# Kernel optimization log

Hardware: AMD Instinct MI355X
Metric: run time of the kernel (lower is better)

Reference implementation:

```python
import jax, jax.numpy as jnp
import numpy as np

B, S, H = 4, 4096, 4096
E, G, TOPK_GROUP, TOP_K = 160, 8, 3, 6
SCALE = 16.0      # routed_scaling_factor (norm_topk_prob=False)
ALPHA = 0.001     # aux_loss_alpha
M = 3             # config.M for communication aux loss


def setup_inputs() -> dict:
    key = jax.random.key(0)
    k1, k2 = jax.random.split(key)
    hidden_states = jax.random.normal(k1, (B, S, H), dtype=jnp.float32)
    # kaiming_uniform_(a=sqrt(5)) on (E, H): bound = 1/sqrt(fan_in)
    bound = 1.0 / np.sqrt(H)
    weight = jax.random.uniform(k2, (E, H), minval=-bound, maxval=bound, dtype=jnp.float32)
    return {"hidden_states": hidden_states, "weight": weight}


def _gate(hidden_states, weight):
    b, s, h = hidden_states.shape
    x = hidden_states.reshape(-1, h).astype(jnp.float32)          # [T, H]
    logits = x @ weight.astype(jnp.float32).T                      # [T, E]
    scores = jax.nn.softmax(logits, axis=-1)
    T = b * s
    # group-limited greedy top-k
    group_scores = scores.reshape(T, G, E // G).max(axis=-1)       # [T, G]
    _, group_idx = jax.lax.top_k(group_scores, TOPK_GROUP)         # [T, topk_group]
    group_mask = jnp.zeros((T, G), scores.dtype).at[
        jnp.arange(T)[:, None], group_idx].set(1.0)                # [T, G]
    score_mask = jnp.repeat(group_mask, E // G, axis=1)            # [T, E]
    tmp_scores = jnp.where(score_mask > 0, scores, 0.0)
    topk_weight, topk_idx = jax.lax.top_k(tmp_scores, TOP_K)       # [T, k]
    topk_weight = topk_weight * SCALE
    # --- aux losses (training, seq_aux=True, alpha>0) ---
    idx_flat = topk_idx.reshape(b, s * TOP_K)                      # [b, s*k]
    counts = jax.vmap(
        lambda idx: jnp.zeros((E,), jnp.float32).at[idx].add(1.0)
    )(idx_flat)                                                    # [b, E]
    ce = counts / (s * TOP_K / E)
    mean_scores = scores.reshape(b, s, E).mean(axis=1)             # [b, E]
    aux_expert = (ce * mean_scores).sum(axis=1).mean() * ALPHA
    ce_g = ce.reshape(b, G, -1).mean(axis=-1)                      # [b, G]
    ms_g = mean_scores.reshape(b, G, -1).mean(axis=-1)             # [b, G]
    aux_device = (ce_g * ms_g).sum(axis=1).mean() * ALPHA
    ce2 = counts.reshape(b, G, -1).sum(axis=-1) / (M * s / G)      # [b, G]
    aux_comm = (ce2 * ms_g).sum(axis=1).mean() * ALPHA
    aux_loss = aux_expert + aux_device + aux_comm
    return topk_idx, topk_weight, aux_loss


def reference(hidden_states, weight):
    return _gate(hidden_states, weight)
```

## Files before the change

kernel.cpp:

```cpp
#include <hip/hip_runtime.h>

typedef _Float16 half8 __attribute__((ext_vector_type(8)));
typedef float f32x4 __attribute__((ext_vector_type(4)));

#define H    4096
#define NE   160
#define BM   64
#define TPB  512
#define NIT  64


__global__ __launch_bounds__(256) void prep_kernel(
    const float* __restrict__ w, _Float16* __restrict__ Wf)
{
    int F    = blockIdx.x * 256 + threadIdx.x;
    int lane = F & 63;
    int t10  = (F >> 6) % 10;
    int ks   = F / 640;
    int e    = t10 * 16 + (lane & 15);
    int k0   = ks * 32 + (lane >> 4) * 8;
    const float* p = w + (size_t)e * H + k0;
    float4 v0 = *(const float4*)p;
    float4 v1 = *(const float4*)(p + 4);
    float vv[8] = {v0.x, v0.y, v0.z, v0.w, v1.x, v1.y, v1.z, v1.w};
    half8 h0, h1;
#pragma unroll
    for (int j = 0; j < 8; ++j) {
        float s = vv[j] * 64.f;
        _Float16 a = (_Float16)s;
        h0[j] = a;
        h1[j] = (_Float16)((s - (float)a) * 2048.f);
    }
    half8* out = (half8*)Wf;
    out[(ks * 20 + t10) * 64 + lane]      = h0;
    out[(ks * 20 + 10 + t10) * 64 + lane] = h1;
}

#define GLOAD_LDS(SRC, DST)                                                    \
    __builtin_amdgcn_global_load_lds(                                          \
        (const __attribute__((address_space(1))) unsigned int*)(SRC),          \
        (__attribute__((address_space(3))) unsigned int*)(DST), 16, 0, 0)

#define LOADX(U0, U1, KIDX)                                                    \
    do {                                                                       \
        U0 = *(const float4*)(xp + (size_t)(KIDX) * 32);                       \
        U1 = *(const float4*)(xp + (size_t)(KIDX) * 32 + 4);                   \
    } while (0)

#define CONVERT(U0, U1)                                                        \
    do {                                                                       \
        float v0=U0.x, v1=U0.y, v2=U0.z, v3=U0.w;                              \
        float v4=U1.x, v5=U1.y, v6=U1.z, v7=U1.w;                              \
        _Float16 h;                                                            \
        h=(_Float16)v0; a0[0]=h; a1[0]=(_Float16)((v0-(float)h)*2048.f);       \
        h=(_Float16)v1; a0[1]=h; a1[1]=(_Float16)((v1-(float)h)*2048.f);       \
        h=(_Float16)v2; a0[2]=h; a1[2]=(_Float16)((v2-(float)h)*2048.f);       \
        h=(_Float16)v3; a0[3]=h; a1[3]=(_Float16)((v3-(float)h)*2048.f);       \
        h=(_Float16)v4; a0[4]=h; a1[4]=(_Float16)((v4-(float)h)*2048.f);       \
        h=(_Float16)v5; a0[5]=h; a1[5]=(_Float16)((v5-(float)h)*2048.f);       \
        h=(_Float16)v6; a0[6]=h; a1[6]=(_Float16)((v6-(float)h)*2048.f);       \
        h=(_Float16)v7; a0[7]=h; a1[7]=(_Float16)((v7-(float)h)*2048.f);       \
    } while (0)

#define KSTEP(LKS, U0, U1)                                                     \
    do {                                                                       \
        const half8* _B = (const half8*)s_stage + cur * 2560 + (LKS) * 1280    \
                          + nh * 5 * 64 + lane;                                \
        half8 bb0[5], bb1[5];                                                  \
        _Pragma("unroll")                                                      \
        for (int _t = 0; _t < 5; ++_t) {                                       \
            bb0[_t] = _B[_t * 64];                                             \
            bb1[_t] = _B[640 + _t * 64];                                       \
        }                                                                      \
        CONVERT(U0, U1);                                                       \
        _Pragma("unroll")                                                      \
        for (int _t = 0; _t < 5; ++_t) {                                       \
            accH[_t] = __builtin_amdgcn_mfma_f32_16x16x32_f16(a0, bb0[_t], accH[_t], 0, 0, 0); \
            accL[_t] = __builtin_amdgcn_mfma_f32_16x16x32_f16(a1, bb0[_t], accL[_t], 0, 0, 0); \
            accL[_t] = __builtin_amdgcn_mfma_f32_16x16x32_f16(a0, bb1[_t], accL[_t], 0, 0, 0); \
        }                                                                      \
    } while (0)

__global__ __launch_bounds__(TPB) void gate_kernel(
    const float* __restrict__ x, const _Float16* __restrict__ Wf,
    float* __restrict__ outIdx, float* __restrict__ outW,
    float* __restrict__ gcnt, float* __restrict__ gssum)
{
    __shared__ __align__(16) _Float16 s_stage[2 * 2560 * 8];
    __shared__ float s_mx[BM], s_inv[BM];
    __shared__ int   s_cnt[NE];
    float* s_log = (float*)s_stage;

    const int tid  = threadIdx.x;
    const int lane = tid & 63;
    const int wv   = tid >> 6;
    const int mh   = wv >> 1;
    const int nh   = wv & 1;
    const int row0 = blockIdx.x * BM;
    const int rowl = mh * 16 + (lane & 15);
    const int kq   = (lane >> 4) * 8;

    if (tid < NE) s_cnt[tid] = 0;

    f32x4 accH[5], accL[5];
#pragma unroll
    for (int t = 0; t < 5; ++t) { accH[t] = (f32x4){0,0,0,0}; accL[t] = (f32x4){0,0,0,0}; }

    const float* xp = x + (size_t)(row0 + rowl) * H + kq;

    half8 a0, a1;
    float4 uA0, uA1, uB0, uB1, uC0, uC1, uD0, uD1, uE0, uE1, uF0, uF1;

    {
        const _Float16* src = Wf + (size_t)tid * 8;
        _Float16*       dst = s_stage + (size_t)tid * 8;
#pragma unroll
        for (int i = 0; i < 5; ++i)
            GLOAD_LDS(src + i * 4096, dst + i * 4096);
    }
    LOADX(uA0, uA1, 0);
    LOADX(uB0, uB1, 1);
    LOADX(uC0, uC1, 2);
    LOADX(uD0, uD1, 3);
    asm volatile("s_waitcnt vmcnt(0)" ::: "memory");
    __syncthreads();

    int cur = 0;
    for (int it = 0; it < NIT; ++it) {
        if (it + 1 < NIT) {
            const _Float16* src = Wf + ((size_t)(it + 1) * 2560 + tid) * 8;
            _Float16*       dst = s_stage + ((size_t)(cur ^ 1) * 2560 + tid) * 8;
#pragma unroll
            for (int i = 0; i < 5; ++i)
                GLOAD_LDS(src + i * 4096, dst + i * 4096);
        }
        {
            const int kpa = ((it + 2) * 2) & (2 * NIT - 1);
            LOADX(uE0, uE1, kpa);
            LOADX(uF0, uF1, kpa + 1);
        }
        KSTEP(0, uA0, uA1);
        KSTEP(1, uB0, uB1);

        asm volatile("s_waitcnt vmcnt(0)" ::: "memory");
        __syncthreads();

        uA0 = uC0; uA1 = uC1; uB0 = uD0; uB1 = uD1;
        uC0 = uE0; uC1 = uE1; uD0 = uF0; uD1 = uF1;
        cur ^= 1;
    }

    const int crow  = mh * 16 + (lane >> 4) * 4;
    const int ccol0 = nh * 80 + (lane & 15);
#pragma unroll
    for (int t = 0; t < 5; ++t)
#pragma unroll
        for (int r = 0; r < 4; ++r)
            s_log[(crow + r) * 161 + ccol0 + t * 16] =
                (accH[t][r] + accL[t][r] * (1.0f / 2048.f)) * (1.0f / 64.f);
    __syncthreads();

    if (tid < BM) {
        const float* L = &s_log[tid * 161];
        float gmax[8];
        float mx = -3.4e38f;
#pragma unroll
        for (int g = 0; g < 8; ++g) {
            float m = L[g * 20];
            for (int j = 1; j < 20; ++j) m = fmaxf(m, L[g * 20 + j]);
            gmax[g] = m;
            mx = fmaxf(mx, m);
        }
        float sum = 0.f;
        for (int e = 0; e < NE; ++e) sum += __expf(L[e] - mx);
        float inv = 1.0f / sum;
        s_mx[tid]  = mx;
        s_inv[tid] = inv;

        unsigned sel = 0;
        float pv = 3.4e38f; int pi = -1;
        for (int it = 0; it < 3; ++it) {
            float bv = -3.4e38f; int bi = 0;
            for (int g = 0; g < 8; ++g) {
                float v = gmax[g];
                bool below = (v < pv) || (v == pv && g > pi);
                if (below && v > bv) { bv = v; bi = g; }
            }
            sel |= 1u << bi;
            pv = bv; pi = bi;
        }

        const int tok = row0 + tid;
        float pv2 = 3.4e38f; int pi2 = -1;
        for (int it = 0; it < 6; ++it) {
            float bv = -3.4e38f; int bi = 0;
            for (int g = 0; g < 8; ++g) {
                if (!((sel >> g) & 1u)) continue;
                for (int j = 0; j < 20; ++j) {
                    int e = g * 20 + j;
                    float v = L[e];
                    bool below = (v < pv2) || (v == pv2 && e > pi2);
                    if (below && v > bv) { bv = v; bi = e; }
                }
            }
            pv2 = bv; pi2 = bi;
            outIdx[(size_t)tok * 6 + it] = (float)bi;
            outW[(size_t)tok * 6 + it]   = __expf(bv - mx) * inv * 16.0f;
            atomicAdd(&s_cnt[bi], 1);
        }
    }
    __syncthreads();

    if (tid < NE) {
        float ss = 0.f;
        for (int t2 = 0; t2 < BM; ++t2)
            ss += __expf(s_log[t2 * 161 + tid] - s_mx[t2]) * s_inv[t2];
        const int b = row0 >> 12;
        atomicAdd(&gssum[b * NE + tid], ss);
        atomicAdd(&gcnt[b * NE + tid], (float)s_cnt[tid]);
    }
}

__global__ __launch_bounds__(64) void aux_kernel(
    const float* __restrict__ gcnt, const float* __restrict__ gssum,
    float* __restrict__ out)
{
    const int lane = threadIdx.x;
    float part = 0.f;
    if (lane < 32) {
        const int b = lane >> 3, g = lane & 7;
        const float* cn = gcnt  + b * NE + g * 20;
        const float* sm = gssum + b * NE + g * 20;
        float s1 = 0.f, sc = 0.f, sms = 0.f;
        for (int j = 0; j < 20; ++j) {
            float ce = cn[j] * (1.0f / 153.6f);
            float ms = sm[j] * (1.0f / 4096.0f);
            s1  += ce * ms;
            sc  += cn[j];
            sms += ms;
        }
        float ceg = sc * (1.0f / 153.6f) * (1.0f / 20.0f);
        float msg = sms * (1.0f / 20.0f);
        float ce2 = sc * (1.0f / 1536.0f);
        part = s1 + ceg * msg + ce2 * msg;
    }
#pragma unroll
    for (int off = 32; off > 0; off >>= 1) part += __shfl_down(part, off);
    if (lane == 0) out[0] = part * (0.001f * 0.25f);
}

extern "C" void kernel_launch(void* const* d_in, const int* in_sizes, int n_in,
                              void* d_out, int out_size, void* d_ws, size_t ws_size,
                              hipStream_t stream)
{
    (void)in_sizes; (void)n_in; (void)out_size; (void)ws_size;
    const float* x = (const float*)d_in[0];
    const float* w = (const float*)d_in[1];
    float* out = (float*)d_out;

    _Float16* Wf  = (_Float16*)d_ws;
    float* gcnt  = (float*)(Wf + (size_t)NE * H * 2);
    float* gssum = gcnt + 4 * NE;

    hipMemsetAsync(gcnt, 0, 2 * 4 * NE * sizeof(float), stream);

    prep_kernel<<<(NE * H / 8) / 256, 256, 0, stream>>>(w, Wf);
    gate_kernel<<<16384 / BM, TPB, 0, stream>>>(
        x, Wf, out, out + 98304, gcnt, gssum);
    aux_kernel<<<1, 64, 0, stream>>>(gcnt, gssum, out + 196608);
}
```

Measured before the change: 240.5 us.

## Triple-buffer weight tiles in LDS with prefetch distance two and partial vmcnt waits

Expands the shared-memory staging for the fp16 weight tiles from two buffers to three and issues the weight prefetch two iterations ahead, rotating buffer offsets each iteration. The full `vmcnt(0)` wait plus `__syncthreads` at the end of each step is replaced by a `vmcnt(9)` wait and a raw `s_barrier` at the top of the loop. This lets the current iteration's global loads stay in flight while the MFMA work runs, aiming to hide global memory latency. In exchange it uses more LDS and relies on exact counting of outstanding vector-memory ops. The last two iterations also issue prefetches past the end of the weight buffer.

```diff
diff --git a/kernel.cpp b/kernel.cpp
--- a/kernel.cpp
+++ b/kernel.cpp
@@ -62,9 +62,9 @@
         h=(_Float16)v7; a0[7]=h; a1[7]=(_Float16)((v7-(float)h)*2048.f);       \
     } while (0)
 
-#define KSTEP(LKS, U0, U1)                                                     \
+#define KSTEP(CUR, LKS, U0, U1)                                                \
     do {                                                                       \
-        const half8* _B = (const half8*)s_stage + cur * 2560 + (LKS) * 1280    \
+        const half8* _B = (const half8*)s_stage + (CUR) + (LKS) * 1280         \
                           + nh * 5 * 64 + lane;                                \
         half8 bb0[5], bb1[5];                                                  \
         _Pragma("unroll")                                                      \
@@ -86,7 +86,7 @@
     float* __restrict__ outIdx, float* __restrict__ outW,
     float* __restrict__ gcnt, float* __restrict__ gssum)
 {
-    __shared__ __align__(16) _Float16 s_stage[2 * 2560 * 8];
+    __shared__ __align__(16) _Float16 s_stage[3 * 2560 * 8];
     __shared__ float s_mx[BM], s_inv[BM];
     __shared__ int   s_cnt[NE];
     float* s_log = (float*)s_stage;
@@ -101,6 +101,7 @@
     const int kq   = (lane >> 4) * 8;
 
     if (tid < NE) s_cnt[tid] = 0;
+    __syncthreads();
 
     f32x4 accH[5], accL[5];
 #pragma unroll
@@ -109,46 +110,54 @@
     const float* xp = x + (size_t)(row0 + rowl) * H + kq;
 
     half8 a0, a1;
-    float4 uA0, uA1, uB0, uB1, uC0, uC1, uD0, uD1, uE0, uE1, uF0, uF1;
+    float4 aU0, aU1, aV0, aV1, bU0, bU1, bV0, bV1, cU0, cU1, cV0, cV1;
 
     {
         const _Float16* src = Wf + (size_t)tid * 8;
         _Float16*       dst = s_stage + (size_t)tid * 8;
 #pragma unroll
-        for (int i = 0; i < 5; ++i)
-            GLOAD_LDS(src + i * 4096, dst + i * 4096);
-    }
-    LOADX(uA0, uA1, 0);
-    LOADX(uB0, uB1, 1);
-    LOADX(uC0, uC1, 2);
-    LOADX(uD0, uD1, 3);
+        for (int i = 0; i < 5; ++i) GLOAD_LDS(src + i * 4096, dst + i * 4096);
+    }
+    LOADX(aU0, aU1, 0);
+    LOADX(aV0, aV1, 1);
+    {
+        const _Float16* src = Wf + ((size_t)2560 + tid) * 8;
+        _Float16*       dst = s_stage + ((size_t)2560 + tid) * 8;
+#pragma unroll
+        for (int i = 0; i < 5; ++i) GLOAD_LDS(src + i * 4096, dst + i * 4096);
+    }
+    LOADX(bU0, bU1, 2);
+    LOADX(bV0, bV1, 3);
+
+    int c0 = 0, c1 = 2560, c2 = 5120;
+
+    for (int it = 0; it < NIT; ++it) {
+        asm volatile("s_waitcnt vmcnt(9)" ::: "memory");
+        __builtin_amdgcn_s_barrier();
+
+        {
+            const _Float16* src = Wf + ((size_t)(it + 2) * 2560 + tid) * 8;
+            _Float16*       dst = s_stage + ((size_t)c2 + tid) * 8;
+#pragma unroll
+            for (int i = 0; i < 5; ++i) GLOAD_LDS(src + i * 4096, dst + i * 4096);
+        }
+        {
+            const int kb = (2 * (it + 2)) & (2 * NIT - 1);
+            LOADX(cU0, cU1, kb);
+            LOADX(cV0, cV1, kb + 1);
+        }
+        __builtin_amdgcn_sched_barrier(0);
+
+        KSTEP(c0, 0, aU0, aU1);
+        KSTEP(c0, 1, aV0, aV1);
+
+        aU0 = bU0; aU1 = bU1; aV0 = bV0; aV1 = bV1;
+        bU0 = cU0; bU1 = cU1; bV0 = cV0; bV1 = cV1;
+        int t0 = c0; c0 = c1; c1 = c2; c2 = t0;
+    }
+
     asm volatile("s_waitcnt vmcnt(0)" ::: "memory");
     __syncthreads();
-
-    int cur = 0;
-    for (int it = 0; it < NIT; ++it) {
-        if (it + 1 < NIT) {
-            const _Float16* src = Wf + ((size_t)(it + 1) * 2560 + tid) * 8;
-            _Float16*       dst = s_stage + ((size_t)(cur ^ 1) * 2560 + tid) * 8;
-#pragma unroll
-            for (int i = 0; i < 5; ++i)
-                GLOAD_LDS(src + i * 4096, dst + i * 4096);
-        }
-        {
-            const int kpa = ((it + 2) * 2) & (2 * NIT - 1);
-            LOADX(uE0, uE1, kpa);
-            LOADX(uF0, uF1, kpa + 1);
-        }
-        KSTEP(0, uA0, uA1);
-        KSTEP(1, uB0, uB1);
-
-        asm volatile("s_waitcnt vmcnt(0)" ::: "memory");
-        __syncthreads();
-
-        uA0 = uC0; uA1 = uC1; uB0 = uD0; uB1 = uD1;
-        uC0 = uE0; uC1 = uE1; uD0 = uF0; uD1 = uF1;
-        cur ^= 1;
-    }
 
     const int crow  = mh * 16 + (lane >> 4) * 4;
     const int ccol0 = nh * 80 + (lane & 15);
```

After: 244.2 us. About the same (+1.5%).

## Halve row tile, split K across waves, drop double buffering and x prefetch pipeline

Applied to the files above, without the earlier changes.

Shrinks the block to 32 rows and 256 threads, giving twice as many blocks. The four waves are split two ways on experts and two ways on K, and each wave covers two 16-row groups. The double-buffered LDS staging of weights and the multi-step register prefetch of x are replaced by a single-buffered load, sync, compute loop, and the two K-halves are combined through shared memory at the end. The aim is more parallelism across CUs and lower LDS and register pressure, at the cost of no overlap between loads and MFMA, twice as many weight reloads from L2 overall, and an extra reduction step.

```diff
diff --git a/kernel.cpp b/kernel.cpp
--- a/kernel.cpp
+++ b/kernel.cpp
@@ -5,8 +5,8 @@
 
 #define H    4096
 #define NE   160
-#define BM   64
-#define TPB  512
+#define BM   32
+#define TPB  256
 #define NIT  64
 
 
@@ -40,12 +40,6 @@
     __builtin_amdgcn_global_load_lds(                                          \
         (const __attribute__((address_space(1))) unsigned int*)(SRC),          \
         (__attribute__((address_space(3))) unsigned int*)(DST), 16, 0, 0)
-
-#define LOADX(U0, U1, KIDX)                                                    \
-    do {                                                                       \
-        U0 = *(const float4*)(xp + (size_t)(KIDX) * 32);                       \
-        U1 = *(const float4*)(xp + (size_t)(KIDX) * 32 + 4);                   \
-    } while (0)
 
 #define CONVERT(U0, U1)                                                        \
     do {                                                                       \
@@ -62,31 +56,12 @@
         h=(_Float16)v7; a0[7]=h; a1[7]=(_Float16)((v7-(float)h)*2048.f);       \
     } while (0)
 
-#define KSTEP(LKS, U0, U1)                                                     \
-    do {                                                                       \
-        const half8* _B = (const half8*)s_stage + cur * 2560 + (LKS) * 1280    \
-                          + nh * 5 * 64 + lane;                                \
-        half8 bb0[5], bb1[5];                                                  \
-        _Pragma("unroll")                                                      \
-        for (int _t = 0; _t < 5; ++_t) {                                       \
-            bb0[_t] = _B[_t * 64];                                             \
-            bb1[_t] = _B[640 + _t * 64];                                       \
-        }                                                                      \
-        CONVERT(U0, U1);                                                       \
-        _Pragma("unroll")                                                      \
-        for (int _t = 0; _t < 5; ++_t) {                                       \
-            accH[_t] = __builtin_amdgcn_mfma_f32_16x16x32_f16(a0, bb0[_t], accH[_t], 0, 0, 0); \
-            accL[_t] = __builtin_amdgcn_mfma_f32_16x16x32_f16(a1, bb0[_t], accL[_t], 0, 0, 0); \
-            accL[_t] = __builtin_amdgcn_mfma_f32_16x16x32_f16(a0, bb1[_t], accL[_t], 0, 0, 0); \
-        }                                                                      \
-    } while (0)
-
 __global__ __launch_bounds__(TPB) void gate_kernel(
     const float* __restrict__ x, const _Float16* __restrict__ Wf,
     float* __restrict__ outIdx, float* __restrict__ outW,
     float* __restrict__ gcnt, float* __restrict__ gssum)
 {
-    __shared__ __align__(16) _Float16 s_stage[2 * 2560 * 8];
+    __shared__ __align__(16) _Float16 s_stage[2560 * 8];
     __shared__ float s_mx[BM], s_inv[BM];
     __shared__ int   s_cnt[NE];
     float* s_log = (float*)s_stage;
@@ -94,70 +69,88 @@
     const int tid  = threadIdx.x;
     const int lane = tid & 63;
     const int wv   = tid >> 6;
-    const int mh   = wv >> 1;
     const int nh   = wv & 1;
+    const int kh   = wv >> 1;
     const int row0 = blockIdx.x * BM;
-    const int rowl = mh * 16 + (lane & 15);
+    const int rql  = lane & 15;
     const int kq   = (lane >> 4) * 8;
 
     if (tid < NE) s_cnt[tid] = 0;
 
-    f32x4 accH[5], accL[5];
-#pragma unroll
-    for (int t = 0; t < 5; ++t) { accH[t] = (f32x4){0,0,0,0}; accL[t] = (f32x4){0,0,0,0}; }
-
-    const float* xp = x + (size_t)(row0 + rowl) * H + kq;
-
-    half8 a0, a1;
-    float4 uA0, uA1, uB0, uB1, uC0, uC1, uD0, uD1, uE0, uE1, uF0, uF1;
-
-    {
-        const _Float16* src = Wf + (size_t)tid * 8;
-        _Float16*       dst = s_stage + (size_t)tid * 8;
-#pragma unroll
-        for (int i = 0; i < 5; ++i)
-            GLOAD_LDS(src + i * 4096, dst + i * 4096);
-    }
-    LOADX(uA0, uA1, 0);
-    LOADX(uB0, uB1, 1);
-    LOADX(uC0, uC1, 2);
-    LOADX(uD0, uD1, 3);
-    asm volatile("s_waitcnt vmcnt(0)" ::: "memory");
-    __syncthreads();
-
-    int cur = 0;
+    f32x4 accH[2][5], accL[2][5];
+#pragma unroll
+    for (int g = 0; g < 2; ++g)
+#pragma unroll
+        for (int t = 0; t < 5; ++t) { accH[g][t] = (f32x4){0,0,0,0}; accL[g][t] = (f32x4){0,0,0,0}; }
+
+    const float* xp0 = x + (size_t)(row0 + rql) * H + kh * 32 + kq;
+    const float* xp1 = xp0 + (size_t)16 * H;
+    const int sbase = kh * 1280 + nh * 5 * 64 + lane;
+
     for (int it = 0; it < NIT; ++it) {
-        if (it + 1 < NIT) {
-            const _Float16* src = Wf + ((size_t)(it + 1) * 2560 + tid) * 8;
-            _Float16*       dst = s_stage + ((size_t)(cur ^ 1) * 2560 + tid) * 8;
-#pragma unroll
-            for (int i = 0; i < 5; ++i)
-                GLOAD_LDS(src + i * 4096, dst + i * 4096);
-        }
+        __syncthreads();
+
         {
-            const int kpa = ((it + 2) * 2) & (2 * NIT - 1);
-            LOADX(uE0, uE1, kpa);
-            LOADX(uF0, uF1, kpa + 1);
-        }
-        KSTEP(0, uA0, uA1);
-        KSTEP(1, uB0, uB1);
-
-        asm volatile("s_waitcnt vmcnt(0)" ::: "memory");
+            const _Float16* srcH = Wf + ((size_t)it * 2560 + tid) * 8;
+            _Float16*       dstH = s_stage + (size_t)tid * 8;
+#pragma unroll
+            for (int i = 0; i < 10; ++i)
+                GLOAD_LDS(srcH + i * 2048, dstH + i * 2048);
+        }
+        float4 u00 = *(const float4*)(xp0 + (size_t)it * 64);
+        float4 u01 = *(const float4*)(xp0 + (size_t)it * 64 + 4);
+        float4 u10 = *(const float4*)(xp1 + (size_t)it * 64);
+        float4 u11 = *(const float4*)(xp1 + (size_t)it * 64 + 4);
+
         __syncthreads();
 
-        uA0 = uC0; uA1 = uC1; uB0 = uD0; uB1 = uD1;
-        uC0 = uE0; uC1 = uE1; uD0 = uF0; uD1 = uF1;
-        cur ^= 1;
-    }
-
-    const int crow  = mh * 16 + (lane >> 4) * 4;
+        const half8* B = (const half8*)s_stage + sbase;
+        half8 b0[5], b1[5];
+#pragma unroll
+        for (int t = 0; t < 5; ++t) { b0[t] = B[t * 64]; b1[t] = B[640 + t * 64]; }
+
+        half8 a0, a1;
+        CONVERT(u00, u01);
+#pragma unroll
+        for (int t = 0; t < 5; ++t) {
+            accH[0][t] = __builtin_amdgcn_mfma_f32_16x16x32_f16(a0, b0[t], accH[0][t], 0, 0, 0);
+            accL[0][t] = __builtin_amdgcn_mfma_f32_16x16x32_f16(a1, b0[t], accL[0][t], 0, 0, 0);
+            accL[0][t] = __builtin_amdgcn_mfma_f32_16x16x32_f16(a0, b1[t], accL[0][t], 0, 0, 0);
+        }
+        CONVERT(u10, u11);
+#pragma unroll
+        for (int t = 0; t < 5; ++t) {
+            accH[1][t] = __builtin_amdgcn_mfma_f32_16x16x32_f16(a0, b0[t], accH[1][t], 0, 0, 0);
+            accL[1][t] = __builtin_amdgcn_mfma_f32_16x16x32_f16(a1, b0[t], accL[1][t], 0, 0, 0);
+            accL[1][t] = __builtin_amdgcn_mfma_f32_16x16x32_f16(a0, b1[t], accL[1][t], 0, 0, 0);
+        }
+    }
+
+    __syncthreads();
+
+    const int crow  = (lane >> 4) * 4;
     const int ccol0 = nh * 80 + (lane & 15);
-#pragma unroll
-    for (int t = 0; t < 5; ++t)
-#pragma unroll
-        for (int r = 0; r < 4; ++r)
-            s_log[(crow + r) * 161 + ccol0 + t * 16] =
-                (accH[t][r] + accL[t][r] * (1.0f / 2048.f)) * (1.0f / 64.f);
+    if (kh == 0) {
+#pragma unroll
+        for (int g = 0; g < 2; ++g)
+#pragma unroll
+            for (int t = 0; t < 5; ++t)
+#pragma unroll
+                for (int r = 0; r < 4; ++r)
+                    s_log[(g * 16 + crow + r) * 161 + ccol0 + t * 16] =
+                        (accH[g][t][r] + accL[g][t][r] * (1.0f / 2048.f)) * (1.0f / 64.f);
+    }
+    __syncthreads();
+    if (kh == 1) {
+#pragma unroll
+        for (int g = 0; g < 2; ++g)
+#pragma unroll
+            for (int t = 0; t < 5; ++t)
+#pragma unroll
+                for (int r = 0; r < 4; ++r)
+                    s_log[(g * 16 + crow + r) * 161 + ccol0 + t * 16] +=
+                        (accH[g][t][r] + accL[g][t][r] * (1.0f / 2048.f)) * (1.0f / 64.f);
+    }
     __syncthreads();
 
     if (tid < BM) {
```

New measurement: 238.1 us. Within noise of the previous version (-1.0%).
